# Performance work log

Hardware: AMD Instinct MI355X
Metric: run time of the kernel (lower is better)

Reference implementation:

```python
import jax, jax.numpy as jnp
import numpy as np

R = 8          # shuffle_rate
HEADS = 4
DIM_HEAD = 64


def setup_inputs() -> dict:
    key = jax.random.key(0)
    k1, k2, k3 = jax.random.split(key, 3)
    dim = 64
    C = dim * R * R            # 4096, token channel dim after unshuffle
    inner = HEADS * DIM_HEAD   # 256
    x = jax.random.normal(k1, (8, dim, 256, 256), dtype=jnp.float32)
    W_qkv = jax.random.normal(k2, (C, 3 * inner), dtype=jnp.float32) * (C ** -0.5)
    W_out = jax.random.normal(k3, (inner, C), dtype=jnp.float32) * (inner ** -0.5)
    b_out = jnp.zeros((C,), dtype=jnp.float32)
    return {"x": x, "W_qkv": W_qkv, "W_out": W_out, "b_out": b_out}


def reference(x, W_qkv, W_out, b_out):
    scale = DIM_HEAD ** -0.5
    B, C0, H0, W0 = x.shape
    h, w = H0 // R, W0 // R
    N = h * w
    C = C0 * R * R
    # PixelUnshuffle: [B,C0,H0,W0] -> [B, C0*R*R, h, w]
    xd = x.reshape(B, C0, h, R, w, R).transpose(0, 1, 3, 5, 2, 4).reshape(B, C, h, w)
    # flatten spatial -> tokens [B, N, C]
    tokens = xd.reshape(B, C, N).transpose(0, 2, 1)
    qkv = tokens @ W_qkv                                   # [B, N, 3*inner]
    q, k, v = jnp.split(qkv, 3, axis=-1)
    def heads(t):  # [B,N,inner] -> [B,H,N,d]
        return t.reshape(B, N, HEADS, DIM_HEAD).transpose(0, 2, 1, 3)
    q, k, v = heads(q), heads(k), heads(v)
    dots = jnp.einsum('bhnd,bhmd->bhnm', q, k) * scale
    attn = jax.nn.softmax(dots, axis=-1)
    out = jnp.einsum('bhnm,bhmd->bhnd', attn, v)
    out = out.transpose(0, 2, 1, 3).reshape(B, N, HEADS * DIM_HEAD)
    y = out @ W_out + b_out                                # [B, N, C]
    y = y.transpose(0, 2, 1).reshape(B, C, h, w)
    # PixelShuffle: [B, C0*R*R, h, w] -> [B, C0, H0, W0]
    y = y.reshape(B, C0, R, R, h, w).transpose(0, 1, 4, 2, 5, 3).reshape(B, C0, H0, W0)
    return y
```

## Files before the change

kernel.cpp:

```cpp
#include <hip/hip_runtime.h>

typedef unsigned short u16;
typedef __attribute__((ext_vector_type(8))) short s16x8;
typedef __attribute__((ext_vector_type(4))) short s16x4;
typedef __attribute__((ext_vector_type(4))) float f32x4;

__device__ __forceinline__ u16 f2bf(float f) {
    unsigned int u;
    __builtin_memcpy(&u, &f, 4);
    unsigned int r = u + 0x7FFFu + ((u >> 16) & 1u);
    return (u16)(r >> 16);
}

__device__ __forceinline__ unsigned int cvt_pk_bf16(float a, float b) {
    unsigned int r;
    asm("v_cvt_pk_bf16_f32 %0, %1, %2" : "=v"(r) : "v"(a), "v"(b));
    return r;
}

__device__ __forceinline__ void gl_lds16(const u16* g, u16* l) {
    __builtin_amdgcn_global_load_lds(
        (const __attribute__((address_space(1))) unsigned int*)g,
        (__attribute__((address_space(3))) unsigned int*)l,
        16, 0, 0);
}

__global__ __launch_bounds__(256) void k_transpose(const float* __restrict__ in,
                                                   u16* __restrict__ out,
                                                   int rows, int cols) {
    __shared__ float tile[64][65];
    int bx = blockIdx.x * 64, by = blockIdx.y * 64;
    int tx = threadIdx.x & 63, ty = threadIdx.x >> 6;
    for (int i = ty; i < 64; i += 4)
        tile[i][tx] = in[(size_t)(by + i) * cols + bx + tx];
    __syncthreads();
    for (int i = ty; i < 64; i += 4)
        out[(size_t)(bx + i) * rows + by + tx] = f2bf(tile[tx][i]);
}

__global__ __launch_bounds__(256) void k_gemm_qkv(const float* __restrict__ x,
                                                  const u16* __restrict__ Bt,
                                                  float* __restrict__ P) {
    const int K = 4096;
    __shared__ u16 As[128 * 64];
    __shared__ u16 Bs[128 * 64];
    const int tid = threadIdx.x;
    const int wave = tid >> 6, lane = tid & 63;
    const int quad = lane >> 4, l15 = lane & 15;
    const int wm = wave >> 1, wn = wave & 1;

    int lin = blockIdx.x;
    int rem = (lin & 7) * 96 + (lin >> 3);
    int tn6 = rem % 6;
    int rq  = rem / 6;
    int z   = rq & 1;
    int tmi = rq >> 1;
    const int tm = tmi * 128, tn = tn6 * 128;

    const float* aptr[4];
#pragma unroll
    for (int t = 0; t < 4; ++t) {
        int cidx = wave * 256 + t * 64 + lane;
        int row = cidx >> 3, kc = cidx & 7;
        int m = tm + row;
        int b = m >> 10, n = m & 1023, yy = n >> 5, xx = n & 31;
        aptr[t] = x + (size_t)b * 4194304 + (size_t)z * 2097152
                    + (yy * 8 + kc) * 256 + xx * 8;
    }

    f32x4 acc[4][4] = {};

    for (int k0 = z * 2048; k0 < (z + 1) * 2048; k0 += 64) {
        float4 va[4][2];
#pragma unroll
        for (int t = 0; t < 4; ++t) {
            const float4* sp = (const float4*)aptr[t];
            va[t][0] = sp[0];
            va[t][1] = sp[1];
            aptr[t] += 65536;
        }
        __syncthreads();
#pragma unroll
        for (int t = 0; t < 4; ++t) {
            int c = wave * 256 + t * 64 + lane;
            int row = c >> 3, kc = c & 7;
            gl_lds16(Bt + (size_t)(tn + row) * K + k0 + kc * 8,
                     Bs + (wave * 256 + t * 64) * 8);
        }
#pragma unroll
        for (int t = 0; t < 4; ++t) {
            int cidx = wave * 256 + t * 64 + lane;
            uint4 pk;
            pk.x = cvt_pk_bf16(va[t][0].x, va[t][0].y);
            pk.y = cvt_pk_bf16(va[t][0].z, va[t][0].w);
            pk.z = cvt_pk_bf16(va[t][1].x, va[t][1].y);
            pk.w = cvt_pk_bf16(va[t][1].z, va[t][1].w);
            *(uint4*)(As + cidx * 8) = pk;
        }
        __syncthreads();
        for (int kk = 0; kk < 64; kk += 32) {
            s16x8 af[4], bf[4];
            for (int i = 0; i < 4; ++i)
                af[i] = *(const s16x8*)(As + (wm * 64 + i * 16 + l15) * 64 + kk + quad * 8);
            for (int j = 0; j < 4; ++j)
                bf[j] = *(const s16x8*)(Bs + (wn * 64 + j * 16 + l15) * 64 + kk + quad * 8);
            for (int i = 0; i < 4; ++i)
                for (int j = 0; j < 4; ++j)
                    acc[i][j] = __builtin_amdgcn_mfma_f32_16x16x32_bf16(af[i], bf[j], acc[i][j], 0, 0, 0);
        }
    }

    float* Pz = P + (size_t)z * 8192 * 768;
    for (int i = 0; i < 4; ++i) {
        int mb = tm + wm * 64 + i * 16 + quad * 4;
        for (int j = 0; j < 4; ++j) {
            int col = tn + wn * 64 + j * 16 + l15;
            for (int r = 0; r < 4; ++r)
                Pz[(size_t)(mb + r) * 768 + col] = acc[i][j][r];
        }
    }
}

__global__ __launch_bounds__(256) void k_qkv_reduce(const float* __restrict__ P,
                                                    u16* __restrict__ Qo,
                                                    u16* __restrict__ Ko,
                                                    u16* __restrict__ Vt) {
    __shared__ u16 tile[64][65];
    const int tid = threadIdx.x;
    const int ct = blockIdx.x, mt = blockIdx.y;
    const int c_l = tid & 63;
    const int col = ct * 64 + c_l;
    const int mbase = mt * 64;
    const float* P1 = P + (size_t)8192 * 768;

    if (ct < 8) {
        int which = col >> 8;
        int h = (col >> 6) & 3, d = col & 63;
        u16* dst = (which == 0) ? Qo : Ko;
        for (int k = 0; k < 16; ++k) {
            int m = mbase + (tid >> 6) + k * 4;
            float v = P[(size_t)m * 768 + col] + P1[(size_t)m * 768 + col];
            int b = m >> 10, n = m & 1023;
            dst[((size_t)((b * 4 + h) * 1024 + n)) * 64 + d] = f2bf(v);
        }
    } else {
        int h = ct - 8;
        int b = mbase >> 10;
        int nbase = mbase & 1023;
        for (int k = 0; k < 16; ++k) {
            int ml = (tid >> 6) + k * 4;
            int m = mbase + ml;
            float v = P[(size_t)m * 768 + col] + P1[(size_t)m * 768 + col];
            tile[ml][c_l] = f2bf(v);
        }
        __syncthreads();
        for (int k = 0; k < 16; ++k) {
            int d = (tid >> 6) + k * 4;
            Vt[((size_t)((b * 4 + h) * 64 + d)) * 1024 + nbase + c_l] = tile[c_l][d];
        }
    }
}

__global__ __launch_bounds__(256) void k_attn(const u16* __restrict__ Qb,
                                              const u16* __restrict__ Kb,
                                              const u16* __restrict__ Vt,
                                              u16* __restrict__ aout) {
    const int bh = blockIdx.y;
    const int q0 = blockIdx.x * 64;
    const int tid = threadIdx.x;
    const int wave = tid >> 6, lane = tid & 63;
    const int quad = lane >> 4, l15 = lane & 15;
    const size_t base = (size_t)bh * 1024 * 64;
    const float scale = 0.125f;

    __shared__ u16 Ks[64 * 64];
    __shared__ u16 Vts[64 * 68];
    __shared__ u16 Ps[4][16 * 64];

    s16x8 aq0, aq1;
    {
        const u16* qp = Qb + base + (size_t)(q0 + wave * 16 + l15) * 64 + quad * 8;
        aq0 = *(const s16x8*)(qp);
        aq1 = *(const s16x8*)(qp + 32);
    }

    float m_i[4], l_i[4];
    f32x4 o[4] = {};
    for (int r = 0; r < 4; ++r) { m_i[r] = -1e30f; l_i[r] = 0.f; }

    const int vrow = tid >> 2, vpart = tid & 3;

    for (int t = 0; t < 16; ++t) {
        __syncthreads();
        for (int e = 0; e < 2; ++e) {
            int s = e * 256 + tid;
            gl_lds16(Kb + base + (size_t)t * 4096 + s * 8, Ks + s * 8);
        }
        {
            const u16* src = Vt + base + (size_t)vrow * 1024 + t * 64 + vpart * 16;
            s16x8 a = *(const s16x8*)(src);
            s16x8 b2 = *(const s16x8*)(src + 8);
            *(s16x8*)(Vts + vrow * 68 + vpart * 16) = a;
            *(s16x8*)(Vts + vrow * 68 + vpart * 16 + 8) = b2;
        }
        __syncthreads();

        f32x4 s4[4];
        for (int j = 0; j < 4; ++j) {
            const u16* kr = Ks + (j * 16 + l15) * 64 + quad * 8;
            s16x8 b0 = *(const s16x8*)(kr);
            s16x8 b1 = *(const s16x8*)(kr + 32);
            f32x4 c = {};
            c = __builtin_amdgcn_mfma_f32_16x16x32_bf16(aq0, b0, c, 0, 0, 0);
            c = __builtin_amdgcn_mfma_f32_16x16x32_bf16(aq1, b1, c, 0, 0, 0);
            s4[j] = c;
        }

        for (int r = 0; r < 4; ++r) {
            float sv0 = s4[0][r] * scale, sv1 = s4[1][r] * scale;
            float sv2 = s4[2][r] * scale, sv3 = s4[3][r] * scale;
            float mt = fmaxf(fmaxf(sv0, sv1), fmaxf(sv2, sv3));
            for (int off = 1; off < 16; off <<= 1)
                mt = fmaxf(mt, __shfl_xor(mt, off, 64));
            float mn = fmaxf(m_i[r], mt);
            float alpha = __expf(m_i[r] - mn);
            m_i[r] = mn;
            float p0 = __expf(sv0 - mn), p1 = __expf(sv1 - mn);
            float p2 = __expf(sv2 - mn), p3 = __expf(sv3 - mn);
            u16* pw = Ps[wave] + (quad * 4 + r) * 64 + l15;
            pw[0]  = f2bf(p0);
            pw[16] = f2bf(p1);
            pw[32] = f2bf(p2);
            pw[48] = f2bf(p3);
            float rs = p0 + p1 + p2 + p3;
            for (int off = 1; off < 16; off <<= 1)
                rs += __shfl_xor(rs, off, 64);
            l_i[r] = l_i[r] * alpha + rs;
            for (int dt = 0; dt < 4; ++dt) o[dt][r] *= alpha;
        }

        for (int kk = 0; kk < 64; kk += 32) {
            s16x8 pf = *(const s16x8*)(Ps[wave] + l15 * 64 + kk + quad * 8);
            for (int dt = 0; dt < 4; ++dt) {
                const u16* vr = Vts + (dt * 16 + l15) * 68 + kk + quad * 8;
                s16x4 v0 = *(const s16x4*)(vr);
                s16x4 v1 = *(const s16x4*)(vr + 4);
                s16x8 vf;
                vf[0] = v0[0]; vf[1] = v0[1]; vf[2] = v0[2]; vf[3] = v0[3];
                vf[4] = v1[0]; vf[5] = v1[1]; vf[6] = v1[2]; vf[7] = v1[3];
                o[dt] = __builtin_amdgcn_mfma_f32_16x16x32_bf16(pf, vf, o[dt], 0, 0, 0);
            }
        }
    }

    int b = bh >> 2, h = bh & 3;
    float rl[4];
    for (int r = 0; r < 4; ++r) rl[r] = 1.0f / l_i[r];
    for (int dt = 0; dt < 4; ++dt)
        for (int r = 0; r < 4; ++r) {
            int qrow = q0 + wave * 16 + quad * 4 + r;
            aout[((size_t)(b) * 1024 + qrow) * 256 + h * 64 + dt * 16 + l15] =
                f2bf(o[dt][r] * rl[r]);
        }
}

__global__ __launch_bounds__(256) void k_gemm_out(const u16* __restrict__ A,
                                                  const u16* __restrict__ Bt,
                                                  const float* __restrict__ bias,
                                                  float* __restrict__ out) {
    const int K = 256;
    __shared__ u16 As[128 * 64];
    __shared__ u16 Bs[128 * 64];
    const int tid = threadIdx.x;
    const int wave = tid >> 6, lane = tid & 63;
    const int quad = lane >> 4, l15 = lane & 15;
    const int wm = wave >> 1, wn = wave & 1;
    const int tm = blockIdx.y * 128, tn = blockIdx.x * 128;

    f32x4 acc[4][4] = {};

    for (int k0 = 0; k0 < K; k0 += 64) {
        __syncthreads();
        for (int t = 0; t < 4; ++t) {
            int c = wave * 256 + t * 64 + lane;
            int row = c >> 3, kc = c & 7;
            gl_lds16(A + (size_t)(tm + row) * K + k0 + kc * 8,
                     As + (wave * 256 + t * 64) * 8);
        }
        for (int t = 0; t < 4; ++t) {
            int c = wave * 256 + t * 64 + lane;
            int row = c >> 3, kc = c & 7;
            gl_lds16(Bt + (size_t)(tn + row) * K + k0 + kc * 8,
                     Bs + (wave * 256 + t * 64) * 8);
        }
        __syncthreads();
        for (int kk = 0; kk < 64; kk += 32) {
            s16x8 af[4], bf[4];
            for (int i = 0; i < 4; ++i)
                af[i] = *(const s16x8*)(As + (wm * 64 + i * 16 + l15) * 64 + kk + quad * 8);
            for (int j = 0; j < 4; ++j)
                bf[j] = *(const s16x8*)(Bs + (wn * 64 + j * 16 + l15) * 64 + kk + quad * 8);
            for (int i = 0; i < 4; ++i)
                for (int j = 0; j < 4; ++j)
                    acc[i][j] = __builtin_amdgcn_mfma_f32_16x16x32_bf16(af[i], bf[j], acc[i][j], 0, 0, 0);
        }
    }

    for (int i = 0; i < 4; ++i) {
        int mb = tm + wm * 64 + i * 16 + quad * 4;
        for (int j = 0; j < 4; ++j) {
            int col = tn + wn * 64 + j * 16 + l15;
            float bb = bias[col];
            int c0 = col >> 6, r1 = (col >> 3) & 7, r2 = col & 7;
            for (int r = 0; r < 4; ++r) {
                int m = mb + r;
                int b = m >> 10, n = m & 1023, yy = n >> 5, xx = n & 31;
                size_t oidx = ((size_t)((b * 64 + c0) * 256 + yy * 8 + r1)) * 256 + xx * 8 + r2;
                out[oidx] = acc[i][j][r] + bb;
            }
        }
    }
}

extern "C" void kernel_launch(void* const* d_in, const int* in_sizes, int n_in,
                              void* d_out, int out_size, void* d_ws, size_t ws_size,
                              hipStream_t stream) {
    (void)in_sizes; (void)n_in; (void)out_size; (void)ws_size;
    const float* x    = (const float*)d_in[0];
    const float* Wqkv = (const float*)d_in[1];
    const float* Wout = (const float*)d_in[2];
    const float* bout = (const float*)d_in[3];
    float* out = (float*)d_out;

    u16* ws     = (u16*)d_ws;
    u16* wqkvT  = ws;
    u16* woutT  = wqkvT + 3145728;
    u16* Qb     = woutT + 1048576;
    u16* Kb     = Qb + 2097152;
    u16* Vtb    = Kb + 2097152;
    u16* aoutb  = Vtb + 2097152;
    float* Pp   = (float*)(aoutb + 2097152);

    k_transpose<<<dim3(12, 64), 256, 0, stream>>>(Wqkv, wqkvT, 4096, 768);
    k_transpose<<<dim3(64, 4), 256, 0, stream>>>(Wout, woutT, 256, 4096);
    k_gemm_qkv<<<dim3(768, 1, 1), 256, 0, stream>>>(x, wqkvT, Pp);
    k_qkv_reduce<<<dim3(12, 128), 256, 0, stream>>>(Pp, Qb, Kb, Vtb);
    k_attn<<<dim3(16, 32), 256, 0, stream>>>(Qb, Kb, Vtb, aoutb);
    k_gemm_out<<<dim3(32, 64), 256, 0, stream>>>(aoutb, woutT, bout, out);
}
```

Before: 474.9 us.

## Prefetch next A tile into registers and swizzle A LDS layout

The fp32 activation loads for the next K step are issued right after the barrier, so they overlap the MFMA work of the current step instead of stalling at the top of the loop. The thread-to-element mapping is changed so consecutive threads read contiguous 32-byte chunks of the unshuffled image rows, which should improve global coalescing. An XOR swizzle is applied to the A tile in LDS to reduce bank conflicts on both the write and the fragment reads. The cost is more live registers for the prefetched data, which may lower occupancy.

```diff
diff --git a/kernel.cpp b/kernel.cpp
--- a/kernel.cpp
+++ b/kernel.cpp
@@ -57,28 +57,31 @@
     int tmi = rq >> 1;
     const int tm = tmi * 128, tn = tn6 * 128;
 
-    const float* aptr[4];
+    const int b   = tm >> 10;
+    const int yy0 = (tm & 1023) >> 5;
+    const float* asrc = x + ((size_t)(b * 64 + z * 32)) * 65536 + yy0 * 2048 + tid * 8;
+
+    u16* dstA[4];
 #pragma unroll
     for (int t = 0; t < 4; ++t) {
-        int cidx = wave * 256 + t * 64 + lane;
-        int row = cidx >> 3, kc = cidx & 7;
-        int m = tm + row;
-        int b = m >> 10, n = m & 1023, yy = n >> 5, xx = n & 31;
-        aptr[t] = x + (size_t)b * 4194304 + (size_t)z * 2097152
-                    + (yy * 8 + kc) * 256 + xx * 8;
+        int row = t * 32 + (tid & 31);
+        int r1  = (tid >> 5) & 7;
+        int byteoff = (row * 128 + r1 * 16) ^ ((tid & 7) << 4);
+        dstA[t] = (u16*)((char*)As + byteoff);
+    }
+
+    float4 va[4][2];
+#pragma unroll
+    for (int t = 0; t < 4; ++t) {
+        const float4* sp = (const float4*)(asrc + t * 2048);
+        va[t][0] = sp[0];
+        va[t][1] = sp[1];
     }
 
     f32x4 acc[4][4] = {};
 
-    for (int k0 = z * 2048; k0 < (z + 1) * 2048; k0 += 64) {
-        float4 va[4][2];
-#pragma unroll
-        for (int t = 0; t < 4; ++t) {
-            const float4* sp = (const float4*)aptr[t];
-            va[t][0] = sp[0];
-            va[t][1] = sp[1];
-            aptr[t] += 65536;
-        }
+    for (int it = 0; it < 32; ++it) {
+        int k0 = z * 2048 + it * 64;
         __syncthreads();
 #pragma unroll
         for (int t = 0; t < 4; ++t) {
@@ -89,19 +92,30 @@
         }
 #pragma unroll
         for (int t = 0; t < 4; ++t) {
-            int cidx = wave * 256 + t * 64 + lane;
             uint4 pk;
             pk.x = cvt_pk_bf16(va[t][0].x, va[t][0].y);
             pk.y = cvt_pk_bf16(va[t][0].z, va[t][0].w);
             pk.z = cvt_pk_bf16(va[t][1].x, va[t][1].y);
             pk.w = cvt_pk_bf16(va[t][1].z, va[t][1].w);
-            *(uint4*)(As + cidx * 8) = pk;
-        }
-        __syncthreads();
+            *(uint4*)dstA[t] = pk;
+        }
+        __syncthreads();
+        if (it < 31) {
+            asrc += 65536;
+#pragma unroll
+            for (int t = 0; t < 4; ++t) {
+                const float4* sp = (const float4*)(asrc + t * 2048);
+                va[t][0] = sp[0];
+                va[t][1] = sp[1];
+            }
+        }
         for (int kk = 0; kk < 64; kk += 32) {
             s16x8 af[4], bf[4];
-            for (int i = 0; i < 4; ++i)
-                af[i] = *(const s16x8*)(As + (wm * 64 + i * 16 + l15) * 64 + kk + quad * 8);
+            for (int i = 0; i < 4; ++i) {
+                int row = wm * 64 + i * 16 + l15;
+                int byteoff = (row * 128 + kk * 2 + quad * 16) ^ ((l15 & 7) << 4);
+                af[i] = *(const s16x8*)((const char*)As + byteoff);
+            }
             for (int j = 0; j < 4; ++j)
                 bf[j] = *(const s16x8*)(Bs + (wn * 64 + j * 16 + l15) * 64 + kk + quad * 8);
             for (int i = 0; i < 4; ++i)
```

Result: faster. 413.0 us (-13.0%).
